# Kernel optimization log

Measured on AMD Instinct MI355X. Metric: run time of the kernel, lower is better.

The kernel has to match this reference:

```python
import jax, jax.numpy as jnp
import numpy as np

EPS = 1e-5

def _point_batch_norm(x, gamma, beta):
    # BatchNorm1d over channel dim of (B, N, C): stats over (B, N), biased var (training mode)
    mu = jnp.mean(x, axis=(0, 1))
    var = jnp.var(x, axis=(0, 1))
    return (x - mu) * jax.lax.rsqrt(var + EPS) * gamma + beta

def setup_inputs() -> dict:
    key = jax.random.key(0)
    ks = jax.random.split(key, 10)
    B, M, N, K = 4, 16384, 32768, 16
    C, Cs, O = 64, 64, 64
    curr_coords = jax.random.normal(ks[0], (B, M, 3), jnp.float32)
    curr_feat = jax.random.normal(ks[1], (B, M, C), jnp.float32)
    skip_coords = jax.random.normal(ks[2], (B, N, 3), jnp.float32)
    skip_feat = jax.random.normal(ks[3], (B, N, Cs), jnp.float32)
    upsampling_idxs = jax.random.randint(ks[4], (B, N, K), 0, M, jnp.int64)
    s1 = 1.0 / np.sqrt(C)
    s2 = 1.0 / np.sqrt(Cs)
    W1 = jax.random.uniform(ks[5], (C, O), jnp.float32, -s1, s1)
    b1 = jax.random.uniform(ks[6], (O,), jnp.float32, -s1, s1)
    W2 = jax.random.uniform(ks[7], (Cs, O), jnp.float32, -s2, s2)
    b2 = jax.random.uniform(ks[8], (O,), jnp.float32, -s2, s2)
    g1 = jnp.ones((O,), jnp.float32); beta1 = jnp.zeros((O,), jnp.float32)
    g2 = jnp.ones((O,), jnp.float32); beta2 = jnp.zeros((O,), jnp.float32)
    return {
        "curr_coords": curr_coords, "curr_feat": curr_feat,
        "skip_coords": skip_coords, "skip_feat": skip_feat,
        "upsampling_idxs": upsampling_idxs,
        "W1": W1, "b1": b1, "g1": g1, "beta1": beta1,
        "W2": W2, "b2": b2, "g2": g2, "beta2": beta2,
    }

def reference(curr_coords, curr_feat, skip_coords, skip_feat, upsampling_idxs,
              W1, b1, g1, beta1, W2, b2, g2, beta2):
    # Gather K-NN neighbor features per skip point: (B, N, K, C), then max over K
    gathered = jax.vmap(lambda f, i: f[i])(curr_feat, upsampling_idxs)
    pooled = jnp.max(gathered, axis=2)  # (B, N, C)
    # proj: Linear -> PointBatchNorm -> ReLU
    h = jax.nn.relu(_point_batch_norm(pooled @ W1 + b1, g1, beta1))
    # proj_skip on skip features
    hs = jax.nn.relu(_point_batch_norm(skip_feat @ W2 + b2, g2, beta2))
    return jnp.concatenate([skip_coords, h, hs], axis=-1)  # (B, N, 3 + 2*O)
```

## Files before the change

kernel.cpp:

```cpp
#include <hip/hip_runtime.h>
#include <hip/hip_bf16.h>

#define BB 4
#define MM 16384
#define NN 32768
#define KK 16
#define ROWS (BB * NN)
#define OUTW 131
#define RPW 32
#define A_BLOCKS (ROWS / (RPW * 4))

__global__ __launch_bounds__(256) void k_pool_proj(
    const float* __restrict__ cf, const int* __restrict__ idxs,
    const float* __restrict__ scoord,
    const float* __restrict__ W1, const float* __restrict__ b1,
    float* __restrict__ out, float* __restrict__ acc)
{
    __shared__ float pool[4][64];
    __shared__ float lsum[64], lsq[64];
    const int lane = threadIdx.x & 63;
    const int wv   = threadIdx.x >> 6;
    if (threadIdx.x < 64) { lsum[threadIdx.x] = 0.f; lsq[threadIdx.x] = 0.f; }
    __syncthreads();

    float w[64];
#pragma unroll
    for (int c = 0; c < 64; ++c) w[c] = W1[c * 64 + lane];
    const float bias = b1[lane];

    float psum = 0.f, psq = 0.f;
    const int gw = blockIdx.x * 4 + wv;
    for (int r0 = 0; r0 < RPW; ++r0) {
        const int r = gw * RPW + r0;
        const int b = r >> 15;
        int mi = 0;
        if (lane < KK) mi = idxs[r * KK + lane];
        float pmax = -3.402823466e38f;
#pragma unroll
        for (int k = 0; k < KK; ++k) {
            const int m = __shfl(mi, k);
            pmax = fmaxf(pmax, cf[(((b << 14) + m) << 6) + lane]);
        }
        pool[wv][lane] = pmax;
        __builtin_amdgcn_wave_barrier();

        float y = bias;
#pragma unroll
        for (int c = 0; c < 64; ++c) y = fmaf(pool[wv][c], w[c], y);
        __builtin_amdgcn_wave_barrier();

        const size_t ob = (size_t)r * OUTW;
        out[ob + 3 + lane] = y;
        if (lane < 3) out[ob + lane] = scoord[r * 3 + lane];
        psum += y; psq += y * y;
    }
    atomicAdd(&lsum[lane], psum);
    atomicAdd(&lsq[lane], psq);
    __syncthreads();
    if (threadIdx.x < 64) {
        atomicAdd(&acc[threadIdx.x],      lsum[threadIdx.x]);
        atomicAdd(&acc[64 + threadIdx.x], lsq[threadIdx.x]);
    }
}

__global__ __launch_bounds__(256) void k_skip_proj(
    const float* __restrict__ sf,
    const float* __restrict__ W2, const float* __restrict__ b2,
    float* __restrict__ out, float* __restrict__ acc)
{
    __shared__ float srow[4][64];
    __shared__ float lsum[64], lsq[64];
    const int lane = threadIdx.x & 63;
    const int wv   = threadIdx.x >> 6;
    if (threadIdx.x < 64) { lsum[threadIdx.x] = 0.f; lsq[threadIdx.x] = 0.f; }
    __syncthreads();

    float w[64];
#pragma unroll
    for (int c = 0; c < 64; ++c) w[c] = W2[c * 64 + lane];
    const float bias = b2[lane];

    float psum = 0.f, psq = 0.f;
    const int gw = blockIdx.x * 4 + wv;
    for (int r0 = 0; r0 < RPW; ++r0) {
        const int r = gw * RPW + r0;
        srow[wv][lane] = sf[(size_t)r * 64 + lane];
        __builtin_amdgcn_wave_barrier();

        float y = bias;
#pragma unroll
        for (int c = 0; c < 64; ++c) y = fmaf(srow[wv][c], w[c], y);
        __builtin_amdgcn_wave_barrier();

        const size_t ob = (size_t)r * OUTW;
        out[ob + 67 + lane] = y;
        psum += y; psq += y * y;
    }
    atomicAdd(&lsum[lane], psum);
    atomicAdd(&lsq[lane], psq);
    __syncthreads();
    if (threadIdx.x < 64) {
        atomicAdd(&acc[128 + threadIdx.x], lsum[threadIdx.x]);
        atomicAdd(&acc[192 + threadIdx.x], lsq[threadIdx.x]);
    }
}

__global__ void k_stats(float* __restrict__ ws,
                        const float* __restrict__ g1, const float* __restrict__ be1,
                        const float* __restrict__ g2, const float* __restrict__ be2)
{
    const int o = threadIdx.x;
    const float inv = 1.0f / (float)ROWS;
    float m1 = ws[o] * inv;
    float v1 = ws[64 + o] * inv - m1 * m1;
    float a1 = g1[o] * rsqrtf(v1 + 1e-5f);
    ws[256 + o] = a1;
    ws[384 + o] = be1[o] - m1 * a1;
    float m2 = ws[128 + o] * inv;
    float v2 = ws[192 + o] * inv - m2 * m2;
    float a2 = g2[o] * rsqrtf(v2 + 1e-5f);
    ws[256 + 64 + o] = a2;
    ws[384 + 64 + o] = be2[o] - m2 * a2;
}

__global__ __launch_bounds__(256) void k_finalize(float* __restrict__ out,
                                                  const float* __restrict__ ws)
{
    const size_t T  = (size_t)gridDim.x * blockDim.x;
    const size_t t0 = (size_t)blockIdx.x * blockDim.x + threadIdx.x;
#pragma unroll
    for (int i = 0; i < 4; ++i) {
        const size_t e = t0 + (size_t)i * T;
        const size_t r = e >> 7;
        const int    j = (int)(e & 127);
        const size_t ad = r * OUTW + 3 + j;
        const float v = out[ad];
        out[ad] = fmaxf(fmaf(v, ws[256 + j], ws[384 + j]), 0.f);
    }
}

extern "C" void kernel_launch(void* const* d_in, const int* in_sizes, int n_in,
                              void* d_out, int out_size, void* d_ws, size_t ws_size,
                              hipStream_t stream)
{
    const float* cf     = (const float*)d_in[1];
    const float* scoord = (const float*)d_in[2];
    const float* sf     = (const float*)d_in[3];
    const int*   idxs   = (const int*)  d_in[4];
    const float* W1     = (const float*)d_in[5];
    const float* b1     = (const float*)d_in[6];
    const float* g1     = (const float*)d_in[7];
    const float* be1    = (const float*)d_in[8];
    const float* W2     = (const float*)d_in[9];
    const float* b2     = (const float*)d_in[10];
    const float* g2     = (const float*)d_in[11];
    const float* be2    = (const float*)d_in[12];
    float* out = (float*)d_out;
    float* ws  = (float*)d_ws;

    hipMemsetAsync(ws, 0, 256 * sizeof(float), stream);
    k_pool_proj<<<A_BLOCKS, 256, 0, stream>>>(cf, idxs, scoord, W1, b1, out, ws);
    k_skip_proj<<<A_BLOCKS, 256, 0, stream>>>(sf, W2, b2, out, ws);
    k_stats<<<1, 64, 0, stream>>>(ws, g1, be1, g2, be2);
    k_finalize<<<16384, 256, 0, stream>>>(out, ws);
}
```

Before: 289.7 us.

## Fuse pool and skip projections into one kernel with XCD-aware batch mapping

Merges the pooled-feature projection and the skip-feature projection into a single kernel, so each wave handles both halves of its rows and the kernel launch count drops by one. Blocks are remapped so that blocks landing on the same XCD (blockIdx mod 8) work on the same batch, which is meant to keep each batch's gathered curr_feat slice resident in that XCD's L2. The finalize kernel processes 8 elements per thread with half the blocks. In exchange each block does more serial work, and W2 must be reloaded into registers partway through the kernel.

```diff
diff --git a/kernel.cpp b/kernel.cpp
--- a/kernel.cpp
+++ b/kernel.cpp
@@ -10,98 +10,84 @@
 #define RPW 32
 #define A_BLOCKS (ROWS / (RPW * 4))
 
-__global__ __launch_bounds__(256) void k_pool_proj(
+__global__ __launch_bounds__(256) void k_fused_proj(
     const float* __restrict__ cf, const int* __restrict__ idxs,
-    const float* __restrict__ scoord,
+    const float* __restrict__ scoord, const float* __restrict__ sf,
     const float* __restrict__ W1, const float* __restrict__ b1,
+    const float* __restrict__ W2, const float* __restrict__ b2,
     float* __restrict__ out, float* __restrict__ acc)
 {
-    __shared__ float pool[4][64];
-    __shared__ float lsum[64], lsq[64];
+    __shared__ float tile[4][64];
+    __shared__ float ls1[64], lq1[64], ls2[64], lq2[64];
     const int lane = threadIdx.x & 63;
     const int wv   = threadIdx.x >> 6;
-    if (threadIdx.x < 64) { lsum[threadIdx.x] = 0.f; lsq[threadIdx.x] = 0.f; }
+    if (threadIdx.x < 64) {
+        ls1[threadIdx.x] = 0.f; lq1[threadIdx.x] = 0.f;
+        ls2[threadIdx.x] = 0.f; lq2[threadIdx.x] = 0.f;
+    }
     __syncthreads();
 
+    const int xcd   = blockIdx.x & 7;
+    const int batch = xcd >> 1;
+    const int blkIB = ((blockIdx.x >> 3) << 1) | (xcd & 1);
+    const int gw    = blkIB * 4 + wv;
+    const int rbase = (batch << 15) + gw * RPW;
+
     float w[64];
+    float psum, psq;
+
 #pragma unroll
     for (int c = 0; c < 64; ++c) w[c] = W1[c * 64 + lane];
-    const float bias = b1[lane];
-
-    float psum = 0.f, psq = 0.f;
-    const int gw = blockIdx.x * 4 + wv;
+    float bias = b1[lane];
+    psum = 0.f; psq = 0.f;
     for (int r0 = 0; r0 < RPW; ++r0) {
-        const int r = gw * RPW + r0;
-        const int b = r >> 15;
+        const int r = rbase + r0;
         int mi = 0;
         if (lane < KK) mi = idxs[r * KK + lane];
         float pmax = -3.402823466e38f;
 #pragma unroll
         for (int k = 0; k < KK; ++k) {
             const int m = __shfl(mi, k);
-            pmax = fmaxf(pmax, cf[(((b << 14) + m) << 6) + lane]);
+            pmax = fmaxf(pmax, cf[(((batch << 14) + m) << 6) + lane]);
         }
-        pool[wv][lane] = pmax;
+        tile[wv][lane] = pmax;
         __builtin_amdgcn_wave_barrier();
-
         float y = bias;
 #pragma unroll
-        for (int c = 0; c < 64; ++c) y = fmaf(pool[wv][c], w[c], y);
+        for (int c = 0; c < 64; ++c) y = fmaf(tile[wv][c], w[c], y);
         __builtin_amdgcn_wave_barrier();
-
         const size_t ob = (size_t)r * OUTW;
         out[ob + 3 + lane] = y;
         if (lane < 3) out[ob + lane] = scoord[r * 3 + lane];
         psum += y; psq += y * y;
     }
-    atomicAdd(&lsum[lane], psum);
-    atomicAdd(&lsq[lane], psq);
+    atomicAdd(&ls1[lane], psum);
+    atomicAdd(&lq1[lane], psq);
+
+#pragma unroll
+    for (int c = 0; c < 64; ++c) w[c] = W2[c * 64 + lane];
+    bias = b2[lane];
+    psum = 0.f; psq = 0.f;
+    for (int r0 = 0; r0 < RPW; ++r0) {
+        const int r = rbase + r0;
+        tile[wv][lane] = sf[(size_t)r * 64 + lane];
+        __builtin_amdgcn_wave_barrier();
+        float y = bias;
+#pragma unroll
+        for (int c = 0; c < 64; ++c) y = fmaf(tile[wv][c], w[c], y);
+        __builtin_amdgcn_wave_barrier();
+        out[(size_t)r * OUTW + 67 + lane] = y;
+        psum += y; psq += y * y;
+    }
+    atomicAdd(&ls2[lane], psum);
+    atomicAdd(&lq2[lane], psq);
+
     __syncthreads();
     if (threadIdx.x < 64) {
-        atomicAdd(&acc[threadIdx.x],      lsum[threadIdx.x]);
-        atomicAdd(&acc[64 + threadIdx.x], lsq[threadIdx.x]);
-    }
-}
-
-__global__ __launch_bounds__(256) void k_skip_proj(
-    const float* __restrict__ sf,
-    const float* __restrict__ W2, const float* __restrict__ b2,
-    float* __restrict__ out, float* __restrict__ acc)
-{
-    __shared__ float srow[4][64];
-    __shared__ float lsum[64], lsq[64];
-    const int lane = threadIdx.x & 63;
-    const int wv   = threadIdx.x >> 6;
-    if (threadIdx.x < 64) { lsum[threadIdx.x] = 0.f; lsq[threadIdx.x] = 0.f; }
-    __syncthreads();
-
-    float w[64];
-#pragma unroll
-    for (int c = 0; c < 64; ++c) w[c] = W2[c * 64 + lane];
-    const float bias = b2[lane];
-
-    float psum = 0.f, psq = 0.f;
-    const int gw = blockIdx.x * 4 + wv;
-    for (int r0 = 0; r0 < RPW; ++r0) {
-        const int r = gw * RPW + r0;
-        srow[wv][lane] = sf[(size_t)r * 64 + lane];
-        __builtin_amdgcn_wave_barrier();
-
-        float y = bias;
-#pragma unroll
-        for (int c = 0; c < 64; ++c) y = fmaf(srow[wv][c], w[c], y);
-        __builtin_amdgcn_wave_barrier();
-
-        const size_t ob = (size_t)r * OUTW;
-        out[ob + 67 + lane] = y;
-        psum += y; psq += y * y;
-    }
-    atomicAdd(&lsum[lane], psum);
-    atomicAdd(&lsq[lane], psq);
-    __syncthreads();
-    if (threadIdx.x < 64) {
-        atomicAdd(&acc[128 + threadIdx.x], lsum[threadIdx.x]);
-        atomicAdd(&acc[192 + threadIdx.x], lsq[threadIdx.x]);
+        atomicAdd(&acc[threadIdx.x],       ls1[threadIdx.x]);
+        atomicAdd(&acc[64 + threadIdx.x],  lq1[threadIdx.x]);
+        atomicAdd(&acc[128 + threadIdx.x], ls2[threadIdx.x]);
+        atomicAdd(&acc[192 + threadIdx.x], lq2[threadIdx.x]);
     }
 }
 
@@ -129,7 +115,7 @@
     const size_t T  = (size_t)gridDim.x * blockDim.x;
     const size_t t0 = (size_t)blockIdx.x * blockDim.x + threadIdx.x;
 #pragma unroll
-    for (int i = 0; i < 4; ++i) {
+    for (int i = 0; i < 8; ++i) {
         const size_t e = t0 + (size_t)i * T;
         const size_t r = e >> 7;
         const int    j = (int)(e & 127);
@@ -159,8 +145,8 @@
     float* ws  = (float*)d_ws;
 
     hipMemsetAsync(ws, 0, 256 * sizeof(float), stream);
-    k_pool_proj<<<A_BLOCKS, 256, 0, stream>>>(cf, idxs, scoord, W1, b1, out, ws);
-    k_skip_proj<<<A_BLOCKS, 256, 0, stream>>>(sf, W2, b2, out, ws);
+    k_fused_proj<<<A_BLOCKS, 256, 0, stream>>>(cf, idxs, scoord, sf,
+                                               W1, b1, W2, b2, out, ws);
     k_stats<<<1, 64, 0, stream>>>(ws, g1, be1, g2, be2);
-    k_finalize<<<16384, 256, 0, stream>>>(out, ws);
+    k_finalize<<<8192, 256, 0, stream>>>(out, ws);
 }
```

After: 433.9 us. +49.8%, slower.
